# Kernel tuning notes

Hardware: AMD Instinct MI355X
Metric: run time of the kernel (lower is better)

## Reference

```python
import jax, jax.numpy as jnp
import numpy as np

NVIEW = 6
N = 6400        # nodes (hardcoded in source: torch.empty(6400, 6))
D = 2048        # input_dim
H = 512         # hidden_dim
C = 256         # common_dim
E = 204800      # edges per view (avg degree 32)


def spmm(h, src, dst, val):
    # sparse_adj @ h : gather source rows, scale by edge value, scatter-add to dst
    msg = val[:, None] * h[src]              # [E, F]
    return jax.ops.segment_sum(msg, dst, num_segments=N)


def setup_inputs() -> dict:
    key = jax.random.key(0)
    ks = jax.random.split(key, 12)
    x = jax.random.normal(ks[0], (NVIEW, N, D), dtype=jnp.float32)
    adj_src = jax.random.randint(ks[1], (NVIEW, E), 0, N, dtype=jnp.int32)
    adj_dst = jax.random.randint(ks[2], (NVIEW, E), 0, N, dtype=jnp.int32)
    # normalized-adjacency-like positive values, scaled ~1/degree to keep activations sane
    adj_val = jax.random.uniform(ks[3], (NVIEW, E), dtype=jnp.float32) / 32.0
    # glorot-ish scaling
    Wb = jax.random.normal(ks[4], (NVIEW, D, H), dtype=jnp.float32) / np.sqrt(D)
    Wo = jax.random.normal(ks[5], (NVIEW, H, H), dtype=jnp.float32) / np.sqrt(H)
    Wf = jax.random.normal(ks[6], (NVIEW, H, H), dtype=jnp.float32) / np.sqrt(H)
    Wc0 = jax.random.normal(ks[7], (D, C), dtype=jnp.float32) / np.sqrt(D)
    Wc1 = jax.random.normal(ks[8], (C, C), dtype=jnp.float32) / np.sqrt(C)
    Wc2 = jax.random.normal(ks[9], (C, C), dtype=jnp.float32) / np.sqrt(C)
    gate_w = jax.random.normal(ks[10], (NVIEW, NVIEW, H + C), dtype=jnp.float32) / np.sqrt(H + C)
    gate_b = jax.random.normal(ks[11], (NVIEW, NVIEW), dtype=jnp.float32) * 0.01
    return {"x": x, "adj_val": adj_val, "Wb": Wb, "Wo": Wo, "Wf": Wf,
            "Wc0": Wc0, "Wc1": Wc1, "Wc2": Wc2, "gate_w": gate_w, "gate_b": gate_b,
            "adj_src": adj_src, "adj_dst": adj_dst}


def reference(x, adj_val, Wb, Wo, Wf, Wc0, Wc1, Wc2, gate_w, gate_b, adj_src, adj_dst):
    zs = []
    for v in range(NVIEW):
        src, dst, val = adj_src[v], adj_dst[v], adj_val[v]
        # view-specific 3-layer GCN (relu, relu, identity)
        hidden = jax.nn.relu(spmm(x[v] @ Wb[v], src, dst, val))   # [N, H]
        mid    = jax.nn.relu(spmm(hidden @ Wo[v], src, dst, val)) # [N, H]
        final  = spmm(mid @ Wf[v], src, dst, val)                 # [N, H]
        z_v = (hidden + mid + final) / 3.0                        # layer_agg == 'mean'
        # shared common 3-layer GCN
        c = jax.nn.relu(spmm(x[v] @ Wc0, src, dst, val))          # [N, C]
        c = jax.nn.relu(spmm(c @ Wc1, src, dst, val))
        c = jax.nn.relu(spmm(c @ Wc2, src, dst, val))
        zs.append(jnp.concatenate([c, z_v], axis=1))              # [N, C+H]
    Z = jnp.stack(zs, axis=0)                                     # [V, N, C+H]
    # gate scores: score_k[:, i] = Linear_{k,i}(z_i)
    scores = jnp.einsum('inf,kif->kni', Z, gate_w) + gate_b[:, None, :]  # [V, N, V]
    scores = jax.nn.softmax(scores, axis=-1)
    z_global = jnp.einsum('kni,inf->knf', scores, Z)              # [V, N, C+H]
    return (z_global, Z)
```

## Files before the change

### kernel.cpp

```cpp
#include <hip/hip_runtime.h>
#include <hip/hip_bf16.h>

#define NVIEW 6
#define NN    6400
#define DD    2048
#define HH    512
#define CC    256
#define EE    204800
#define ZF    768

typedef __bf16 bf16x8 __attribute__((ext_vector_type(8)));
typedef __bf16 bf16x4 __attribute__((ext_vector_type(4)));
typedef float  f32x4  __attribute__((ext_vector_type(4)));

__device__ __forceinline__ float b2f(unsigned short u) {
  union { unsigned int i; float f; } c; c.i = ((unsigned int)u) << 16; return c.f;
}

__device__ __forceinline__ void glds16(const void* g, void* l) {
  __builtin_amdgcn_global_load_lds((const __attribute__((address_space(1))) void*)g,
                                   (__attribute__((address_space(3))) void*)l, 16, 0, 0);
}

__global__ void k_hist(const int* __restrict__ dst, int* __restrict__ hist) {
  int e = blockIdx.x * 256 + threadIdx.x;
  int v = blockIdx.y;
  if (e < EE) atomicAdd(&hist[v * NN + dst[(size_t)v * EE + e]], 1);
}

__global__ __launch_bounds__(1024) void k_scan(const int* __restrict__ hist,
                                               int* __restrict__ rp) {
  int v = blockIdx.x;
  const int* h = hist + v * NN;
  int* r = rp + v * (NN + 1);
  __shared__ int part[1024];
  int t = threadIdx.x;
  const int CH = 7;
  int base = t * CH;
  int loc[CH];
  int s = 0;
#pragma unroll
  for (int i = 0; i < CH; i++) {
    int idx = base + i;
    int val = (idx < NN) ? h[idx] : 0;
    loc[i] = s;
    s += val;
  }
  part[t] = s;
  __syncthreads();
  for (int off = 1; off < 1024; off <<= 1) {
    int x = (t >= off) ? part[t - off] : 0;
    __syncthreads();
    part[t] += x;
    __syncthreads();
  }
  int pre = (t == 0) ? 0 : part[t - 1];
#pragma unroll
  for (int i = 0; i < CH; i++) {
    int idx = base + i;
    if (idx < NN) r[idx] = pre + loc[i];
  }
  if (t == 1023) r[NN] = part[1023];
}

__global__ void k_cursor(const int* __restrict__ rp, int* __restrict__ cur) {
  int i = blockIdx.x * 256 + threadIdx.x;
  if (i < NVIEW * NN) {
    int v = i / NN, n = i - v * NN;
    cur[i] = rp[v * (NN + 1) + n];
  }
}

__global__ void k_scatter(const int* __restrict__ src, const int* __restrict__ dstA,
                          const float* __restrict__ val, int* __restrict__ cur,
                          int2* __restrict__ sedge) {
  int e = blockIdx.x * 256 + threadIdx.x;
  int v = blockIdx.y;
  if (e < EE) {
    size_t idx = (size_t)v * EE + e;
    int d = dstA[idx];
    int pos = atomicAdd(&cur[v * NN + d], 1);
    sedge[(size_t)v * EE + pos] = make_int2(src[idx], __float_as_int(val[idx]));
  }
}

__global__ __launch_bounds__(256) void k_cvt(const float* __restrict__ in,
                                             __bf16* __restrict__ out) {
  size_t i = (size_t)blockIdx.x * 256 + threadIdx.x;
  float4 q = ((const float4*)in)[i];
  bf16x4 o;
  o[0] = (__bf16)q.x; o[1] = (__bf16)q.y; o[2] = (__bf16)q.z; o[3] = (__bf16)q.w;
  *(bf16x4*)(out + i * 4) = o;
}

__global__ __launch_bounds__(256) void k_tw(const float* __restrict__ in,
                                            __bf16* __restrict__ out, int K, int N,
                                            size_t inSB, size_t outSB) {
  __shared__ float sh[32][33];
  int b = blockIdx.z;
  int k0 = blockIdx.x * 32, n0 = blockIdx.y * 32;
  int tx = threadIdx.x & 31, ty = threadIdx.x >> 5;
  const float* I = in + (size_t)b * inSB;
  __bf16* O = out + (size_t)b * outSB;
#pragma unroll
  for (int r = 0; r < 4; r++)
    sh[ty + r * 8][tx] = I[(size_t)(k0 + ty + r * 8) * N + n0 + tx];
  __syncthreads();
#pragma unroll
  for (int r = 0; r < 4; r++)
    O[(size_t)(n0 + ty + r * 8) * K + k0 + tx] = (__bf16)sh[tx][ty + r * 8];
}

__global__ __launch_bounds__(512, 2) void k_g256(
    const __bf16* __restrict__ A, const __bf16* __restrict__ BT,
    __bf16* __restrict__ C, int K, int Nc, int nbn, int bpv, int wPerView)
{
  __shared__ __bf16 lds[2 * 16384];
  int tid = threadIdx.x, lane = tid & 63, w = tid >> 6;

  int nwg = gridDim.x;
  int q8 = nwg >> 3, r8 = nwg & 7;
  int orig = blockIdx.x;
  int xcd = orig & 7, j = orig >> 3;
  int swz = (xcd < r8 ? xcd * (q8 + 1) : r8 * (q8 + 1) + (xcd - r8) * q8) + j;
  int v = swz / bpv; int rr = swz - v * bpv;
  int bm = rr / nbn; int bn = rr - bm * nbn;

  const __bf16* Av = A + (size_t)v * NN * K + (size_t)(bm * 256) * K;
  const __bf16* Bv = BT + (wPerView ? (size_t)v * Nc * K : 0) + (size_t)(bn * 256) * K;

  f32x4 acc[8][4];
#pragma unroll
  for (int m = 0; m < 8; m++)
#pragma unroll
    for (int n = 0; n < 4; n++) acc[m][n] = (f32x4){0.f, 0.f, 0.f, 0.f};

  const int wr = (w >> 2) * 128, wc = (w & 3) * 64;
  const int gq = lane >> 4, l15 = lane & 15;

  auto stage = [&](int buf, int k0) {
    __bf16* base = lds + buf * 16384;
#pragma unroll
    for (int i = 0; i < 2; ++i) {
      int c = i * 512 + tid;
      int row = c & 255, kkg = c >> 8;
      glds16(Av + (size_t)row * K + k0 + kkg * 8, base + c * 8);
      glds16(Bv + (size_t)row * K + k0 + kkg * 8, base + 8192 + c * 8);
    }
  };

  const int nt = K >> 5;
  stage(0, 0);
  __syncthreads();
  for (int t = 0; t < nt; ++t) {
    if (t + 1 < nt) stage((t + 1) & 1, (t + 1) << 5);
    const __bf16* Ab = lds + (t & 1) * 16384;
    const __bf16* Bb = Ab + 8192;
    bf16x8 aF[8], bF[4];
#pragma unroll
    for (int m = 0; m < 8; m++)
      aF[m] = *(const bf16x8*)&Ab[(gq * 256 + wr + m * 16 + l15) * 8];
#pragma unroll
    for (int n = 0; n < 4; n++)
      bF[n] = *(const bf16x8*)&Bb[(gq * 256 + wc + n * 16 + l15) * 8];
#pragma unroll
    for (int m = 0; m < 8; m++)
#pragma unroll
      for (int n = 0; n < 4; n++)
        acc[m][n] = __builtin_amdgcn_mfma_f32_16x16x32_bf16(aF[m], bF[n], acc[m][n], 0, 0, 0);
    __syncthreads();
  }

  __bf16* Cv = C + (size_t)v * NN * Nc;
#pragma unroll
  for (int m = 0; m < 8; m++) {
    int rbase = bm * 256 + wr + m * 16 + (lane >> 4) * 4;
#pragma unroll
    for (int q = 0; q < 4; q++) {
      __bf16* cp = Cv + (size_t)(rbase + q) * Nc + bn * 256 + wc + l15;
#pragma unroll
      for (int n = 0; n < 4; n++) cp[n * 16] = (__bf16)acc[m][n][q];
    }
  }
}

template <int LDIN, int FOFF, int F, int CHUNKS, int MODE>
__global__ __launch_bounds__(256) void k_spmm(
    const __bf16* __restrict__ in, const int* __restrict__ rp,
    const int2* __restrict__ sedge, void* __restrict__ out,
    const __bf16* __restrict__ h1, const __bf16* __restrict__ h2)
{
  int id = blockIdx.x;
  int s = id & 7, j = id >> 3;
  int ch, v, rowblk;
  if (CHUNKS == 2) {
    ch = s >> 2; int q = s & 3;
    v = j / 400; int t = j - v * 400;
    rowblk = t * 4 + q;
  } else {
    ch = 0;
    v = j / 200; int t = j - v * 200;
    rowblk = t * 8 + s;
  }
  int wid = threadIdx.x >> 6, lane = threadIdx.x & 63;
  int n = rowblk * 4 + wid;
  int f0 = ch * 256 + lane * 4;

  const int* rpv = rp + v * (NN + 1);
  int e = rpv[n], end = rpv[n + 1];
  const int2* ev = sedge + (size_t)v * EE;
  const __bf16* inv = in + (size_t)v * NN * LDIN + FOFF;

  float a0 = 0.f, a1 = 0.f, a2 = 0.f, a3 = 0.f;
  for (; e + 4 <= end; e += 4) {
    int2 e0 = ev[e], e1 = ev[e + 1], e2 = ev[e + 2], e3 = ev[e + 3];
    float w0 = __int_as_float(e0.y), w1 = __int_as_float(e1.y);
    float w2 = __int_as_float(e2.y), w3 = __int_as_float(e3.y);
    ushort4 r0 = *(const ushort4*)(inv + (size_t)e0.x * LDIN + f0);
    ushort4 r1 = *(const ushort4*)(inv + (size_t)e1.x * LDIN + f0);
    ushort4 r2 = *(const ushort4*)(inv + (size_t)e2.x * LDIN + f0);
    ushort4 r3 = *(const ushort4*)(inv + (size_t)e3.x * LDIN + f0);
    a0 += w0 * b2f(r0.x); a1 += w0 * b2f(r0.y); a2 += w0 * b2f(r0.z); a3 += w0 * b2f(r0.w);
    a0 += w1 * b2f(r1.x); a1 += w1 * b2f(r1.y); a2 += w1 * b2f(r1.z); a3 += w1 * b2f(r1.w);
    a0 += w2 * b2f(r2.x); a1 += w2 * b2f(r2.y); a2 += w2 * b2f(r2.z); a3 += w2 * b2f(r2.w);
    a0 += w3 * b2f(r3.x); a1 += w3 * b2f(r3.y); a2 += w3 * b2f(r3.z); a3 += w3 * b2f(r3.w);
  }
  if (e + 2 <= end) {
    int2 e0 = ev[e], e1 = ev[e + 1];
    float w0 = __int_as_float(e0.y), w1 = __int_as_float(e1.y);
    ushort4 r0 = *(const ushort4*)(inv + (size_t)e0.x * LDIN + f0);
    ushort4 r1 = *(const ushort4*)(inv + (size_t)e1.x * LDIN + f0);
    a0 += w0 * b2f(r0.x); a1 += w0 * b2f(r0.y); a2 += w0 * b2f(r0.z); a3 += w0 * b2f(r0.w);
    a0 += w1 * b2f(r1.x); a1 += w1 * b2f(r1.y); a2 += w1 * b2f(r1.z); a3 += w1 * b2f(r1.w);
    e += 2;
  }
  if (e < end) {
    int2 e0 = ev[e];
    float w0 = __int_as_float(e0.y);
    ushort4 r0 = *(const ushort4*)(inv + (size_t)e0.x * LDIN + f0);
    a0 += w0 * b2f(r0.x); a1 += w0 * b2f(r0.y); a2 += w0 * b2f(r0.z); a3 += w0 * b2f(r0.w);
  }

  if (MODE == 0) {
    __bf16* o = (__bf16*)out + ((size_t)v * NN + n) * F + f0;
    bf16x4 ov;
    ov[0] = (__bf16)fmaxf(a0, 0.f); ov[1] = (__bf16)fmaxf(a1, 0.f);
    ov[2] = (__bf16)fmaxf(a2, 0.f); ov[3] = (__bf16)fmaxf(a3, 0.f);
    *(bf16x4*)o = ov;
  } else if (MODE == 1) {
    float* o = (float*)out + ((size_t)v * NN + n) * ZF + f0;
    o[0] = fmaxf(a0, 0.f); o[1] = fmaxf(a1, 0.f);
    o[2] = fmaxf(a2, 0.f); o[3] = fmaxf(a3, 0.f);
  } else {
    const __bf16* hh = h1 + ((size_t)v * NN + n) * 512 + f0;
    const __bf16* mm = h2 + ((size_t)v * NN + n) * 512 + f0;
    ushort4 hu = *(const ushort4*)hh;
    ushort4 mu = *(const ushort4*)mm;
    float* o = (float*)out + ((size_t)v * NN + n) * ZF + CC + f0;
    o[0] = (b2f(hu.x) + b2f(mu.x) + a0) * (1.f / 3.f);
    o[1] = (b2f(hu.y) + b2f(mu.y) + a1) * (1.f / 3.f);
    o[2] = (b2f(hu.z) + b2f(mu.z) + a2) * (1.f / 3.f);
    o[3] = (b2f(hu.w) + b2f(mu.w) + a3) * (1.f / 3.f);
  }
}

__global__ __launch_bounds__(256) void k_gate(
    const float* __restrict__ Z, const float* __restrict__ gw,
    const float* __restrict__ gb, float* __restrict__ zg)
{
  __shared__ float Zl[NVIEW * ZF];
  __shared__ float sred[36];
  __shared__ float pl[36];
  int n = blockIdx.x, tid = threadIdx.x;

  for (int idx = tid; idx < NVIEW * ZF; idx += 256) {
    int i = idx / ZF, f = idx - i * ZF;
    Zl[idx] = Z[((size_t)i * NN + n) * ZF + f];
  }
  if (tid < 36) sred[tid] = 0.f;
  __syncthreads();

  float acc[36];
#pragma unroll
  for (int p = 0; p < 36; p++) acc[p] = 0.f;
#pragma unroll
  for (int q = 0; q < 3; q++) {
    int f = tid + q * 256;
    float zv[NVIEW];
#pragma unroll
    for (int i = 0; i < NVIEW; i++) zv[i] = Zl[i * ZF + f];
#pragma unroll
    for (int k = 0; k < NVIEW; k++)
#pragma unroll
      for (int i = 0; i < NVIEW; i++)
        acc[k * 6 + i] += zv[i] * gw[(k * 6 + i) * ZF + f];
  }
  int lane = tid & 63;
#pragma unroll
  for (int p = 0; p < 36; p++) {
    float x = acc[p];
    x += __shfl_down(x, 32, 64);
    x += __shfl_down(x, 16, 64);
    x += __shfl_down(x, 8, 64);
    x += __shfl_down(x, 4, 64);
    x += __shfl_down(x, 2, 64);
    x += __shfl_down(x, 1, 64);
    if (lane == 0) atomicAdd(&sred[p], x);
  }
  __syncthreads();

  if (tid < NVIEW) {
    int k = tid;
    float sc[NVIEW];
    float mx = -1e30f;
#pragma unroll
    for (int i = 0; i < NVIEW; i++) {
      sc[i] = sred[k * 6 + i] + gb[k * 6 + i];
      mx = fmaxf(mx, sc[i]);
    }
    float sum = 0.f;
#pragma unroll
    for (int i = 0; i < NVIEW; i++) { sc[i] = __expf(sc[i] - mx); sum += sc[i]; }
    float inv = 1.f / sum;
#pragma unroll
    for (int i = 0; i < NVIEW; i++) pl[k * 6 + i] = sc[i] * inv;
  }
  __syncthreads();

#pragma unroll
  for (int q = 0; q < 3; q++) {
    int f = tid + q * 256;
    float zv[NVIEW];
#pragma unroll
    for (int i = 0; i < NVIEW; i++) zv[i] = Zl[i * ZF + f];
#pragma unroll
    for (int k = 0; k < NVIEW; k++) {
      float o = 0.f;
#pragma unroll
      for (int i = 0; i < NVIEW; i++) o += pl[k * 6 + i] * zv[i];
      zg[((size_t)k * NN + n) * ZF + f] = o;
    }
  }
}

extern "C" void kernel_launch(void* const* d_in, const int* in_sizes, int n_in,
                              void* d_out, int out_size, void* d_ws, size_t ws_size,
                              hipStream_t stream) {
  const float* x    = (const float*)d_in[0];
  const float* aval = (const float*)d_in[1];
  const float* Wb   = (const float*)d_in[2];
  const float* Wo   = (const float*)d_in[3];
  const float* Wf   = (const float*)d_in[4];
  const float* Wc0  = (const float*)d_in[5];
  const float* Wc1  = (const float*)d_in[6];
  const float* Wc2  = (const float*)d_in[7];
  const float* gw   = (const float*)d_in[8];
  const float* gb   = (const float*)d_in[9];
  const int*   asrc = (const int*)d_in[10];
  const int*   adst = (const int*)d_in[11];

  float* zg = (float*)d_out;
  float* Z  = zg + (size_t)NVIEW * NN * ZF;
  __bf16* xb = (__bf16*)d_out;

  char* w = (char*)d_ws;
  auto alloc = [&](size_t bytes) {
    char* p = w;
    w += (bytes + 255) & ~(size_t)255;
    return p;
  };
  int*    hist  = (int*)alloc((size_t)NVIEW * NN * 4);
  int*    rp    = (int*)alloc((size_t)NVIEW * (NN + 1) * 4);
  int2*   sedge = (int2*)alloc((size_t)NVIEW * EE * 8);
  __bf16* Wfu   = (__bf16*)alloc((size_t)NVIEW * ZF * DD * 2);
  __bf16* WoT   = (__bf16*)alloc((size_t)NVIEW * HH * HH * 2);
  __bf16* WfT   = (__bf16*)alloc((size_t)NVIEW * HH * HH * 2);
  __bf16* Wc1T  = (__bf16*)alloc((size_t)CC * CC * 2);
  __bf16* Wc2T  = (__bf16*)alloc((size_t)CC * CC * 2);
  __bf16* tf768 = (__bf16*)alloc((size_t)NVIEW * NN * ZF * 2);
  __bf16* t512b = (__bf16*)alloc((size_t)NVIEW * NN * HH * 2);
  __bf16* hidb  = (__bf16*)alloc((size_t)NVIEW * NN * HH * 2);
  __bf16* midb  = (__bf16*)alloc((size_t)NVIEW * NN * HH * 2);
  __bf16* tcb   = (__bf16*)alloc((size_t)NVIEW * NN * CC * 2);
  __bf16* cbb   = (__bf16*)alloc((size_t)NVIEW * NN * CC * 2);

  (void)hipMemsetAsync(hist, 0, (size_t)NVIEW * NN * 4, stream);
  k_hist<<<dim3(800, NVIEW), 256, 0, stream>>>(adst, hist);
  k_scan<<<NVIEW, 1024, 0, stream>>>(hist, rp);
  k_cursor<<<150, 256, 0, stream>>>(rp, hist);
  k_scatter<<<dim3(800, NVIEW), 256, 0, stream>>>(asrc, adst, aval, hist, sedge);

  k_cvt<<<76800, 256, 0, stream>>>(x, xb);
  k_tw<<<dim3(64, 16, NVIEW), 256, 0, stream>>>(Wb, Wfu, DD, HH,
                                                (size_t)DD * HH, (size_t)ZF * DD);
  k_tw<<<dim3(64, 8, NVIEW), 256, 0, stream>>>(Wc0, Wfu + (size_t)HH * DD, DD, CC,
                                               0, (size_t)ZF * DD);
  k_tw<<<dim3(16, 16, NVIEW), 256, 0, stream>>>(Wo, WoT, HH, HH,
                                                (size_t)HH * HH, (size_t)HH * HH);
  k_tw<<<dim3(16, 16, NVIEW), 256, 0, stream>>>(Wf, WfT, HH, HH,
                                                (size_t)HH * HH, (size_t)HH * HH);
  k_tw<<<dim3(8, 8, 1), 256, 0, stream>>>(Wc1, Wc1T, CC, CC, 0, 0);
  k_tw<<<dim3(8, 8, 1), 256, 0, stream>>>(Wc2, Wc2T, CC, CC, 0, 0);

  k_g256<<<450, 512, 0, stream>>>(xb, Wfu, tf768, DD, ZF, 3, 75, 1);
  k_spmm<768, 0, 512, 2, 0><<<19200, 256, 0, stream>>>(tf768, rp, sedge, hidb, nullptr, nullptr);
  k_spmm<768, 512, 256, 1, 0><<<9600, 256, 0, stream>>>(tf768, rp, sedge, cbb, nullptr, nullptr);

  k_g256<<<300, 512, 0, stream>>>(hidb, WoT, t512b, HH, HH, 2, 50, 1);
  k_spmm<512, 0, 512, 2, 0><<<19200, 256, 0, stream>>>(t512b, rp, sedge, midb, nullptr, nullptr);
  k_g256<<<150, 512, 0, stream>>>(cbb, Wc1T, tcb, CC, CC, 1, 25, 0);
  k_spmm<256, 0, 256, 1, 0><<<9600, 256, 0, stream>>>(tcb, rp, sedge, cbb, nullptr, nullptr);
  k_g256<<<300, 512, 0, stream>>>(midb, WfT, t512b, HH, HH, 2, 50, 1);
  k_spmm<512, 0, 512, 2, 2><<<19200, 256, 0, stream>>>(t512b, rp, sedge, Z, hidb, midb);
  k_g256<<<150, 512, 0, stream>>>(cbb, Wc2T, tcb, CC, CC, 1, 25, 0);
  k_spmm<256, 0, 256, 1, 1><<<9600, 256, 0, stream>>>(tcb, rp, sedge, Z, nullptr, nullptr);

  k_gate<<<NN, 256, 0, stream>>>(Z, gw, gb, zg);
}
```

Baseline: 1.316 ms.

## Restructure GEMM mainloop into 8-phase pipelined schedule with K=64 tiles

Rewrites the 256x256 bf16 GEMM mainloop to use K=64 tiles in a 128KB double buffer. Each iteration is split into eight phases that interleave LDS fragment reads, partial global->LDS staging and half-tile MFMA bursts. The phases are separated by explicit barriers, vmcnt waits and setprio. This aims to hide global-load latency and LDS read latency behind MFMA work. The larger LDS footprint (128KB) likely prevents two workgroups per CU despite launch_bounds(512,2), and the extra barriers add sync overhead.

```diff
diff --git a/kernel.cpp b/kernel.cpp
--- a/kernel.cpp
+++ b/kernel.cpp
@@ -115,7 +115,7 @@
     const __bf16* __restrict__ A, const __bf16* __restrict__ BT,
     __bf16* __restrict__ C, int K, int Nc, int nbn, int bpv, int wPerView)
 {
-  __shared__ __bf16 lds[2 * 16384];
+  __shared__ __bf16 ldsv[65536];
   int tid = threadIdx.x, lane = tid & 63, w = tid >> 6;
 
   int nwg = gridDim.x;
@@ -138,38 +138,87 @@
   const int wr = (w >> 2) * 128, wc = (w & 3) * 64;
   const int gq = lane >> 4, l15 = lane & 15;
 
-  auto stage = [&](int buf, int k0) {
-    __bf16* base = lds + buf * 16384;
-#pragma unroll
-    for (int i = 0; i < 2; ++i) {
-      int c = i * 512 + tid;
-      int row = c & 255, kkg = c >> 8;
-      glds16(Av + (size_t)row * K + k0 + kkg * 8, base + c * 8);
-      glds16(Bv + (size_t)row * K + k0 + kkg * 8, base + 8192 + c * 8);
+#define STAGE_UNIT(Gp, LOFF, KH, KT)                                          \
+  {                                                                           \
+    _Pragma("unroll")                                                         \
+    for (int g2 = 0; g2 < 2; g2++) {                                          \
+      int chunk = (KH) * 1024 + (w + g2 * 8) * 64 + lane;                     \
+      int row_ = chunk & 255, kkg_ = chunk >> 8;                              \
+      glds16(Gp + (size_t)row_ * K + (KT) * 64 + kkg_ * 8,                    \
+             ldsv + (LOFF) + chunk * 8);                                      \
+    }                                                                         \
+  }
+
+#define PH_READS(KK, MH, LOADB)                                               \
+  {                                                                           \
+    _Pragma("unroll")                                                         \
+    for (int m = 0; m < 4; m++)                                               \
+      aF[m] = *(const bf16x8*)&Ab[(((KK) * 4 + gq) * 256 + wr + (MH) * 64 +   \
+                                   m * 16 + l15) * 8];                        \
+    if (LOADB) {                                                              \
+      _Pragma("unroll")                                                       \
+      for (int n = 0; n < 4; n++)                                             \
+        bF[n] = *(const bf16x8*)&Bb[(((KK) * 4 + gq) * 256 + wc + n * 16 +    \
+                                     l15) * 8];                               \
+    }                                                                         \
+  }
+
+#define PH_MFMA(MH)                                                           \
+  {                                                                           \
+    __builtin_amdgcn_s_barrier();                                             \
+    asm volatile("s_waitcnt lgkmcnt(0)" ::: "memory");                        \
+    __builtin_amdgcn_sched_barrier(0);                                        \
+    __builtin_amdgcn_s_setprio(1);                                            \
+    _Pragma("unroll")                                                         \
+    for (int m = 0; m < 4; m++)                                               \
+      _Pragma("unroll")                                                       \
+      for (int n = 0; n < 4; n++)                                             \
+        acc[(MH) * 4 + m][n] = __builtin_amdgcn_mfma_f32_16x16x32_bf16(       \
+            aF[m], bF[n], acc[(MH) * 4 + m][n], 0, 0, 0);                     \
+    __builtin_amdgcn_s_setprio(0);                                            \
+    __builtin_amdgcn_s_barrier();                                             \
+  }
+
+  const int nt = K >> 6;
+  const int ni = nt >> 1;
+
+  STAGE_UNIT(Av, 0,     0, 0);
+  STAGE_UNIT(Bv, 16384, 0, 0);
+  STAGE_UNIT(Av, 0,     1, 0);
+  STAGE_UNIT(Bv, 16384, 1, 0);
+  STAGE_UNIT(Av, 32768, 0, 1);
+  STAGE_UNIT(Bv, 49152, 0, 1);
+  asm volatile("s_waitcnt vmcnt(4)" ::: "memory");
+  __builtin_amdgcn_s_barrier();
+
+  bf16x8 aF[4], bF[4];
+  for (int i = 0; i < ni; ++i) {
+    int t1 = 2 * i + 1, t2 = 2 * i + 2, t3 = 2 * i + 3;
+    bool more = (i + 1 < ni);
+    const __bf16* Ab = ldsv;
+    const __bf16* Bb = ldsv + 16384;
+    PH_READS(0, 0, true);  STAGE_UNIT(Av, 32768, 1, t1);              PH_MFMA(0);
+    PH_READS(0, 1, false); STAGE_UNIT(Bv, 49152, 1, t1);              PH_MFMA(1);
+    PH_READS(1, 0, true);  if (more) STAGE_UNIT(Av, 0,     0, t2);    PH_MFMA(0);
+    PH_READS(1, 1, false); if (more) STAGE_UNIT(Bv, 16384, 0, t2);
+    if (more) asm volatile("s_waitcnt vmcnt(4)" ::: "memory");
+    else      asm volatile("s_waitcnt vmcnt(0)" ::: "memory");
+    PH_MFMA(1);
+    Ab = ldsv + 32768; Bb = ldsv + 49152;
+    PH_READS(0, 0, true);  if (more) STAGE_UNIT(Av, 0,     1, t2);    PH_MFMA(0);
+    PH_READS(0, 1, false); if (more) STAGE_UNIT(Bv, 16384, 1, t2);    PH_MFMA(1);
+    PH_READS(1, 0, true);  if (more) STAGE_UNIT(Av, 32768, 0, t3);    PH_MFMA(0);
+    PH_READS(1, 1, false);
+    if (more) {
+      STAGE_UNIT(Bv, 49152, 0, t3);
+      asm volatile("s_waitcnt vmcnt(4)" ::: "memory");
     }
-  };
-
-  const int nt = K >> 5;
-  stage(0, 0);
-  __syncthreads();
-  for (int t = 0; t < nt; ++t) {
-    if (t + 1 < nt) stage((t + 1) & 1, (t + 1) << 5);
-    const __bf16* Ab = lds + (t & 1) * 16384;
-    const __bf16* Bb = Ab + 8192;
-    bf16x8 aF[8], bF[4];
-#pragma unroll
-    for (int m = 0; m < 8; m++)
-      aF[m] = *(const bf16x8*)&Ab[(gq * 256 + wr + m * 16 + l15) * 8];
-#pragma unroll
-    for (int n = 0; n < 4; n++)
-      bF[n] = *(const bf16x8*)&Bb[(gq * 256 + wc + n * 16 + l15) * 8];
-#pragma unroll
-    for (int m = 0; m < 8; m++)
-#pragma unroll
-      for (int n = 0; n < 4; n++)
-        acc[m][n] = __builtin_amdgcn_mfma_f32_16x16x32_bf16(aF[m], bF[n], acc[m][n], 0, 0, 0);
-    __syncthreads();
-  }
+    PH_MFMA(1);
+  }
+
+#undef STAGE_UNIT
+#undef PH_READS
+#undef PH_MFMA
 
   __bf16* Cv = C + (size_t)v * NN * Nc;
 #pragma unroll
```

Result: faster. 1.246 ms (-5.3%).
